# Performance work log

Hardware: AMD Instinct MI355X
Metric: run time of the kernel (lower is better)

## Reference

```python
import jax, jax.numpy as jnp
import numpy as np

VOCAB = 4  # token alphabet size used in setup_inputs


def setup_inputs() -> dict:
    key = jax.random.key(0)
    k1, k2 = jax.random.split(key)
    xq = jax.random.randint(k1, (8192, 512), 0, VOCAB, dtype=jnp.int32)
    xp = jax.random.randint(k2, (8192, 512), 0, VOCAB, dtype=jnp.int32)
    return {"xq": xq, "xp": xp}


def reference(xq, xp):
    # Pairwise Hamming distance: dists[n, m] = sum_d [xq[n, d] != xp[m, d]].
    # Expressed as D minus the match count, computed as a one-hot GEMM
    # (matches[n,m] = sum_{d,v} 1[xq[n,d]==v] * 1[xp[m,d]==v]) so the whole
    # NxMxD reduction is a single fused contraction instead of the original
    # per-row broadcast-compare loop. Exact in fp32 since counts <= D = 512.
    D = xq.shape[1]
    qh = jax.nn.one_hot(xq, VOCAB, dtype=jnp.float32)  # [N, D, V]
    ph = jax.nn.one_hot(xp, VOCAB, dtype=jnp.float32)  # [M, D, V]
    matches = jnp.einsum('ndv,mdv->nm', qh, ph)        # [N, M]
    return (jnp.float32(D) - matches).astype(jnp.int32)
```

## Files before the change

kernel.cpp:

```cpp
#include <hip/hip_runtime.h>
#include <stdint.h>


#define NROWS 8192
#define THREADS 512

typedef int   v4i  __attribute__((ext_vector_type(4)));
typedef int   v8i  __attribute__((ext_vector_type(8)));
typedef float v16f __attribute__((ext_vector_type(16)));

#define AS1(p) ((const __attribute__((address_space(1))) void*)(p))
#define AS3(p) ((__attribute__((address_space(3))) void*)(p))

__global__ __launch_bounds__(512) void pack_kernel(
    const int* __restrict__ xq, const int* __restrict__ xp,
    uint8_t* __restrict__ qpk, uint8_t* __restrict__ ppk) {
  __shared__ uint8_t lt[64 * 384];
  const int bid = blockIdx.x;
  const int op  = bid & 1;
  const int dh  = (bid >> 1) & 1;
  const int R64 = bid >> 2;
  const int t   = threadIdx.x;
  const int* src = op ? xp : xq;
  uint8_t*   dst = op ? ppk : qpk;
  const int row0 = R64 * 64;
  const int d0   = dh * 256;

  #pragma unroll
  for (int i = 0; i < 8; ++i) {
    const int idx = i * 512 + t;
    const int rl = idx >> 6, q = idx & 63;
    const int4 a = ((const int4*)(src + (size_t)(row0 + rl) * 512 + d0))[q];
    const int tok[4] = {a.x, a.y, a.z, a.w};
    uint32_t n0 = 0, n1 = 0, n2 = 0;
    #pragma unroll
    for (int j = 0; j < 4; ++j) {
      const uint32_t b1 = (tok[j] >> 1) & 1, b0 = tok[j] & 1;
      n0 |= (0x2u | (b1 << 3)) << (4 * j);
      n1 |= (0x2u | (b0 << 3)) << (4 * j);
      n2 |= (0x2u | ((b1 ^ b0) << 3)) << (4 * j);
    }
    uint8_t* p = lt + rl * 384 + (((q >> 3) ^ (rl & 7)) << 4) + (q & 7) * 2;
    *(uint16_t*)(p)       = (uint16_t)n0;
    *(uint16_t*)(p + 128) = (uint16_t)n1;
    *(uint16_t*)(p + 256) = (uint16_t)n2;
  }
  __syncthreads();

  const size_t Rg = R64 >> 2;
  const int rb = (R64 & 3) * 64;
  #pragma unroll
  for (int i = 0; i < 3; ++i) {
    const int o = i * 512 + t;
    const int c = o >> 9, sg = (o >> 6) & 7, rl = o & 63;
    const int kt = c * 2 + dh;
    const uint4 v = *(const uint4*)(lt + rl * 384 + c * 128 + ((sg ^ (rl & 7)) << 4));
    *(uint4*)(dst + (((Rg * 6 + kt) * 8 + sg) * 256 + rb + rl) * 16) = v;
  }
}

__global__ __launch_bounds__(THREADS, 2) void hamming_mfma(
    const uint8_t* __restrict__ Apk, const uint8_t* __restrict__ Bpk,
    int* __restrict__ out) {
  __shared__ __align__(128) uint8_t lds[131072];

  const int t = threadIdx.x, l = t & 63, w = t >> 6;
  const int wr = w >> 2, wc = w & 3;

  const int bid = blockIdx.x;
  const int nid = (bid & 7) * 128 + (bid >> 3);
  const int br = nid >> 5, bc = nid & 31;

  const uint8_t* Abase = Apk + (size_t)br * 196608;
  const uint8_t* Bbase = Bpk + (size_t)bc * 196608;

  const int stoff = w * 1024 + l * 16;
  const int g4   = (l >> 5) * 4096;
  const int aoff = g4 + wr * 2048 + (l & 31) * 16;
  const int boff = g4 + wc * 1024 + (l & 31) * 16;

  v16f acc[4][2] = {};

  #pragma unroll
  for (int p = 0; p < 4; ++p) {
    __builtin_amdgcn_global_load_lds(AS1(Abase + p * 8192 + stoff),
                                     AS3(lds + p * 8192 + stoff), 16, 0, 0);
    __builtin_amdgcn_global_load_lds(AS1(Bbase + p * 8192 + stoff),
                                     AS3(lds + 32768 + p * 8192 + stoff), 16, 0, 0);
  }

  for (int kk = 0; kk < 6; ++kk) {
    const int cur = kk & 1;
    const int ktn = (kk == 5) ? 0 : kk + 1;
    const uint8_t* an = Abase + ktn * 32768;
    const uint8_t* bn = Bbase + ktn * 32768;
    uint8_t* ldsc = lds + cur * 65536;
    uint8_t* ldsn = lds + (cur ^ 1) * 65536;

    #pragma unroll
    for (int p = 0; p < 4; ++p) {
      asm volatile("s_waitcnt vmcnt(6)" ::: "memory");
      __builtin_amdgcn_s_barrier();
      __builtin_amdgcn_global_load_lds(AS1(an + p * 8192 + stoff),
                                       AS3(ldsn + p * 8192 + stoff), 16, 0, 0);
      __builtin_amdgcn_global_load_lds(AS1(bn + p * 8192 + stoff),
                                       AS3(ldsn + 32768 + p * 8192 + stoff), 16, 0, 0);
      const uint8_t* ab = ldsc + p * 8192;
      const uint8_t* bb = ldsc + 32768 + p * 8192;
      v4i af[4], bf[2];
      #pragma unroll
      for (int m = 0; m < 4; ++m) af[m] = *(const v4i*)(ab + aoff + m * 512);
      #pragma unroll
      for (int n = 0; n < 2; ++n) bf[n] = *(const v4i*)(bb + boff + n * 512);
      asm volatile("s_waitcnt lgkmcnt(0)" ::: "memory");
      __builtin_amdgcn_sched_barrier(0);
      __builtin_amdgcn_s_setprio(1);
      #pragma unroll
      for (int m = 0; m < 4; ++m)
        #pragma unroll
        for (int n = 0; n < 2; ++n) {
          const v8i av = (v8i){af[m][0], af[m][1], af[m][2], af[m][3], 0, 0, 0, 0};
          const v8i bv = (v8i){bf[n][0], bf[n][1], bf[n][2], bf[n][3], 0, 0, 0, 0};
          acc[m][n] = __builtin_amdgcn_mfma_scale_f32_32x32x64_f8f6f4(
              av, bv, acc[m][n], 4 , 4 ,
              0, 0x7F7F7F7F, 0, 0x7F7F7F7F);
        }
      __builtin_amdgcn_s_setprio(0);
      __builtin_amdgcn_s_barrier();
    }
  }
  asm volatile("s_waitcnt vmcnt(0)" ::: "memory");

  const int rbase = br * 256 + wr * 128 + 4 * (l >> 5);
  const int cbase = bc * 256 + wc * 64 + (l & 31);
  #pragma unroll
  for (int m = 0; m < 4; ++m)
    #pragma unroll
    for (int n = 0; n < 2; ++n) {
      const int col = cbase + n * 32;
      #pragma unroll
      for (int reg = 0; reg < 16; ++reg) {
        const int orow = rbase + m * 32 + (reg & 3) + 8 * (reg >> 2);
        out[(size_t)orow * NROWS + col] = 512 - (((int)acc[m][n][reg] + 512) >> 2);
      }
    }
}

extern "C" void kernel_launch(void* const* d_in, const int* in_sizes, int n_in,
                              void* d_out, int out_size, void* d_ws, size_t ws_size,
                              hipStream_t stream) {
  const int* xq = (const int*)d_in[0];
  const int* xp = (const int*)d_in[1];
  int* out = (int*)d_out;

  uint8_t* qpk = (uint8_t*)d_ws;
  uint8_t* ppk = qpk + (size_t)NROWS * 768;

  pack_kernel<<<512, 512, 0, stream>>>(xq, xp, qpk, ppk);
  hamming_mfma<<<1024, THREADS, 0, stream>>>(qpk, ppk, out);
}
```

Baseline: 322.7 us.

## Drop LDS staging; load MFMA operands directly from global into registers

Replaces the LDS double-buffered global_load_lds pipeline with direct per-wave global loads into a register-resident prefetch buffer of four k-steps. The block shrinks to 256 threads with a 256x128 tile and twice as many blocks, remapped in an 8x8 grouped order for L2 locality, and output stores become nontemporal. This removes LDS traffic and block-wide barriers, but each wave now reads its operands straight from global/L2, which raises redundant global loads and register pressure.

```diff
diff --git a/kernel.cpp b/kernel.cpp
--- a/kernel.cpp
+++ b/kernel.cpp
@@ -3,14 +3,10 @@
 
 
 #define NROWS 8192
-#define THREADS 512
 
 typedef int   v4i  __attribute__((ext_vector_type(4)));
 typedef int   v8i  __attribute__((ext_vector_type(8)));
 typedef float v16f __attribute__((ext_vector_type(16)));
-
-#define AS1(p) ((const __attribute__((address_space(1))) void*)(p))
-#define AS3(p) ((__attribute__((address_space(3))) void*)(p))
 
 __global__ __launch_bounds__(512) void pack_kernel(
     const int* __restrict__ xq, const int* __restrict__ xp,
@@ -59,80 +55,66 @@
   }
 }
 
-__global__ __launch_bounds__(THREADS, 2) void hamming_mfma(
+__global__ __launch_bounds__(256, 2) void hamming_mfma(
     const uint8_t* __restrict__ Apk, const uint8_t* __restrict__ Bpk,
     int* __restrict__ out) {
-  __shared__ __align__(128) uint8_t lds[131072];
-
   const int t = threadIdx.x, l = t & 63, w = t >> 6;
-  const int wr = w >> 2, wc = w & 3;
+  const int wr = w >> 1, wc = w & 1;
 
   const int bid = blockIdx.x;
-  const int nid = (bid & 7) * 128 + (bid >> 3);
-  const int br = nid >> 5, bc = nid & 31;
+  const int nid = (bid & 7) * 256 + (bid >> 3);
+  const int q = nid & 63, p = nid >> 6;
+  const int br = (p >> 3) * 8 + (q >> 3);
+  const int bc = (p & 7) * 8 + (q & 7);
 
-  const uint8_t* Abase = Apk + (size_t)br * 196608;
-  const uint8_t* Bbase = Bpk + (size_t)bc * 196608;
+  const int g = l >> 5, ll = l & 31;
+  const uint8_t* abase = Apk + (size_t)br * 196608 + g * 4096
+                       + (size_t)(wr * 128 + ll) * 16;
+  const uint8_t* bbase = Bpk + (size_t)(bc >> 1) * 196608 + g * 4096
+                       + (size_t)((bc & 1) * 128 + wc * 64 + ll) * 16;
 
-  const int stoff = w * 1024 + l * 16;
-  const int g4   = (l >> 5) * 4096;
-  const int aoff = g4 + wr * 2048 + (l & 31) * 16;
-  const int boff = g4 + wc * 1024 + (l & 31) * 16;
-
+  v4i af[4][4], bf[4][2];
   v16f acc[4][2] = {};
 
   #pragma unroll
-  for (int p = 0; p < 4; ++p) {
-    __builtin_amdgcn_global_load_lds(AS1(Abase + p * 8192 + stoff),
-                                     AS3(lds + p * 8192 + stoff), 16, 0, 0);
-    __builtin_amdgcn_global_load_lds(AS1(Bbase + p * 8192 + stoff),
-                                     AS3(lds + 32768 + p * 8192 + stoff), 16, 0, 0);
+  for (int i = 0; i < 4; ++i) {
+    #pragma unroll
+    for (int m = 0; m < 4; ++m)
+      af[i][m] = *(const v4i*)(abase + i * 8192 + m * 512);
+    #pragma unroll
+    for (int n = 0; n < 2; ++n)
+      bf[i][n] = *(const v4i*)(bbase + i * 8192 + n * 512);
   }
 
-  for (int kk = 0; kk < 6; ++kk) {
-    const int cur = kk & 1;
-    const int ktn = (kk == 5) ? 0 : kk + 1;
-    const uint8_t* an = Abase + ktn * 32768;
-    const uint8_t* bn = Bbase + ktn * 32768;
-    uint8_t* ldsc = lds + cur * 65536;
-    uint8_t* ldsn = lds + (cur ^ 1) * 65536;
-
+  for (int so = 0; so < 24; so += 4) {
+    const int snext = (so + 4 == 24) ? 0 : so + 4;
+    const uint8_t* pa = abase + snext * 8192;
+    const uint8_t* pb = bbase + snext * 8192;
     #pragma unroll
-    for (int p = 0; p < 4; ++p) {
-      asm volatile("s_waitcnt vmcnt(6)" ::: "memory");
-      __builtin_amdgcn_s_barrier();
-      __builtin_amdgcn_global_load_lds(AS1(an + p * 8192 + stoff),
-                                       AS3(ldsn + p * 8192 + stoff), 16, 0, 0);
-      __builtin_amdgcn_global_load_lds(AS1(bn + p * 8192 + stoff),
-                                       AS3(ldsn + 32768 + p * 8192 + stoff), 16, 0, 0);
-      const uint8_t* ab = ldsc + p * 8192;
-      const uint8_t* bb = ldsc + 32768 + p * 8192;
-      v4i af[4], bf[2];
-      #pragma unroll
-      for (int m = 0; m < 4; ++m) af[m] = *(const v4i*)(ab + aoff + m * 512);
-      #pragma unroll
-      for (int n = 0; n < 2; ++n) bf[n] = *(const v4i*)(bb + boff + n * 512);
-      asm volatile("s_waitcnt lgkmcnt(0)" ::: "memory");
-      __builtin_amdgcn_sched_barrier(0);
-      __builtin_amdgcn_s_setprio(1);
+    for (int i = 0; i < 4; ++i) {
       #pragma unroll
       for (int m = 0; m < 4; ++m)
         #pragma unroll
         for (int n = 0; n < 2; ++n) {
-          const v8i av = (v8i){af[m][0], af[m][1], af[m][2], af[m][3], 0, 0, 0, 0};
-          const v8i bv = (v8i){bf[n][0], bf[n][1], bf[n][2], bf[n][3], 0, 0, 0, 0};
+          const v8i av = (v8i){af[i][m][0], af[i][m][1], af[i][m][2], af[i][m][3],
+                               0, 0, 0, 0};
+          const v8i bv = (v8i){bf[i][n][0], bf[i][n][1], bf[i][n][2], bf[i][n][3],
+                               0, 0, 0, 0};
           acc[m][n] = __builtin_amdgcn_mfma_scale_f32_32x32x64_f8f6f4(
               av, bv, acc[m][n], 4 , 4 ,
               0, 0x7F7F7F7F, 0, 0x7F7F7F7F);
         }
-      __builtin_amdgcn_s_setprio(0);
-      __builtin_amdgcn_s_barrier();
+      #pragma unroll
+      for (int m = 0; m < 4; ++m)
+        af[i][m] = *(const v4i*)(pa + i * 8192 + m * 512);
+      #pragma unroll
+      for (int n = 0; n < 2; ++n)
+        bf[i][n] = *(const v4i*)(pb + i * 8192 + n * 512);
     }
   }
-  asm volatile("s_waitcnt vmcnt(0)" ::: "memory");
 
   const int rbase = br * 256 + wr * 128 + 4 * (l >> 5);
-  const int cbase = bc * 256 + wc * 64 + (l & 31);
+  const int cbase = bc * 128 + wc * 64 + (l & 31);
   #pragma unroll
   for (int m = 0; m < 4; ++m)
     #pragma unroll
@@ -141,7 +123,9 @@
       #pragma unroll
       for (int reg = 0; reg < 16; ++reg) {
         const int orow = rbase + m * 32 + (reg & 3) + 8 * (reg >> 2);
-        out[(size_t)orow * NROWS + col] = 512 - (((int)acc[m][n][reg] + 512) >> 2);
+        __builtin_nontemporal_store(
+            512 - (((int)acc[m][n][reg] + 512) >> 2),
+            &out[(size_t)orow * NROWS + col]);
       }
     }
 }
@@ -157,5 +141,5 @@
   uint8_t* ppk = qpk + (size_t)NROWS * 768;
 
   pack_kernel<<<512, 512, 0, stream>>>(xq, xp, qpk, ppk);
-  hamming_mfma<<<1024, THREADS, 0, stream>>>(qpk, ppk, out);
+  hamming_mfma<<<2048, 256, 0, stream>>>(qpk, ppk, out);
 }
```

Result: slower. 342.1 us (+6.0%).
